# Performance work log

Measured on AMD Instinct MI355X. Metric: run time of the kernel, lower is better.

## Reference

```python
import jax, jax.numpy as jnp
import numpy as np

QMAX = 255.0  # bit=8 unsigned activation range


def ste_round(x):
    # straight-through round: exact integer rounding in fwd, identity grad
    return x + jax.lax.stop_gradient(jnp.round(x) - x)


def conv3x3(x, w, stride=1):
    return jax.lax.conv_general_dilated(
        x, w, window_strides=(stride, stride), padding=((1, 1), (1, 1)),
        dimension_numbers=('NCHW', 'OIHW', 'NCHW'))


def setup_inputs() -> dict:
    key = jax.random.key(0)
    k0, k1, k2 = jax.random.split(key, 3)
    N, C, H, W = 64, 256, 28, 28
    # uint8 activations and int8 (symmetric) weights, stored as integer-valued fp32
    x = jax.random.randint(k0, (N, C, H, W), 0, 256).astype(jnp.float32)
    w1 = jax.random.randint(k1, (C, C, 3, 3), -128, 128).astype(jnp.float32)
    w2 = jax.random.randint(k2, (C, C, 3, 3), -128, 128).astype(jnp.float32)
    f = jnp.float32
    return dict(
        x=x, w1=w1, w2=w2,
        s_x=f(0.05), z_x=f(128.0),
        s_w1=f(0.01), s_conv1=f(0.08), z_conv1=f(120.0),
        s_w2=f(0.01), s_conv2=f(0.07), z_conv2=f(130.0),
        s_add=f(0.09), z_add=f(125.0))


def qconv(x_q, w_q, s_in, z_in, s_w, s_out, z_out, stride=1):
    # integer-arithmetic conv: sum((x - z_in) * w) then requantize
    acc = conv3x3(x_q - z_in, w_q, stride)
    M = s_in * s_w / s_out  # per-cluster requant multiplier (cluster 0)
    return jnp.clip(ste_round(M * acc) + z_out, 0.0, QMAX)


def qadd(a, s_a, z_a, b, s_b, z_b, s_out, z_out):
    # fused dequant of both branches + residual add + requant
    y = (s_a / s_out) * (a - z_a) + (s_b / s_out) * (b - z_b)
    return jnp.clip(ste_round(y) + z_out, 0.0, QMAX)


def reference(x, w1, w2, s_x, z_x, s_w1, s_conv1, z_conv1,
              s_w2, s_conv2, z_conv2, s_add, z_add):
    out = qconv(x, w1, s_x, z_x, s_w1, s_conv1, z_conv1)          # conv1
    out = qconv(out, w2, s_conv1, z_conv1, s_w2, s_conv2, z_conv2)  # conv2
    return qadd(x, s_x, z_x, out, s_conv2, z_conv2, s_add, z_add)   # shortcut
```

## Files before the change

kernel.cpp:

```cpp
#include <hip/hip_runtime.h>
#include <stdint.h>

#define HWP 784
#define NPOS 50176
#define PLN ((size_t)NPOS * 64)
#define SLAB_ROWS 186
#define NCHUNK 2976
#define PAD_OFF 47616

typedef int   int4v   __attribute__((ext_vector_type(4)));
typedef int   int16v  __attribute__((ext_vector_type(16)));
typedef float float4v __attribute__((ext_vector_type(4)));
using as1_cv = const __attribute__((address_space(1))) void;
using as3_v  = __attribute__((address_space(3))) void;

__global__ __launch_bounds__(256) void k_nhwc(const float* __restrict__ x,
                                              int8_t* __restrict__ x8) {
    __shared__ int lA[256 * 15];
    __shared__ __align__(16) int lB[56 * 68];
    const int tid = threadIdx.x;
    const int P0 = blockIdx.x * 56;
    const int n = P0 / HWP;
    const int hw0 = P0 % HWP;
    const float* xb = x + (size_t)n * 256 * HWP + hw0;
#pragma unroll
    for (int k = 0; k < 14; ++k) {
        int e = tid + k * 256;
        int c = e / 14, pq = e % 14;
        float4v v = *(const float4v*)(xb + (size_t)c * HWP + pq * 4);
        int b0 = ((int)v[0] - 128) & 255;
        int b1 = ((int)v[1] - 128) & 255;
        int b2 = ((int)v[2] - 128) & 255;
        int b3 = ((int)v[3] - 128) & 255;
        lA[c * 15 + pq] = b0 | (b1 << 8) | (b2 << 16) | (b3 << 24);
    }
    __syncthreads();
#pragma unroll
    for (int k = 0; k < 4; ++k) {
        int u = tid + k * 256;
        if (u < 896) {
            int cg = u / 14, pq = u % 14;
            int d0 = lA[(cg * 4 + 0) * 15 + pq];
            int d1 = lA[(cg * 4 + 1) * 15 + pq];
            int d2 = lA[(cg * 4 + 2) * 15 + pq];
            int d3 = lA[(cg * 4 + 3) * 15 + pq];
#pragma unroll
            for (int j = 0; j < 4; ++j) {
                int sh = j * 8;
                int o = ((d0 >> sh) & 255) | (((d1 >> sh) & 255) << 8)
                      | (((d2 >> sh) & 255) << 16) | (((d3 >> sh) & 255) << 24);
                lB[(pq * 4 + j) * 68 + cg] = o;
            }
        }
    }
    __syncthreads();
#pragma unroll
    for (int k = 0; k < 4; ++k) {
        int ch = tid + k * 256;
        if (ch < 896) {
            int g = ch / 224, rem = ch % 224;
            int pos = rem >> 2, c4 = rem & 3;
            int4v val = *(const int4v*)&lB[pos * 68 + g * 16 + c4 * 4];
            *(int4v*)(x8 + (size_t)g * PLN + (size_t)(P0 + pos) * 64 + c4 * 16) = val;
        }
    }
}

__global__ __launch_bounds__(256) void k_w_prep(const float* __restrict__ wa,
                                                const float* __restrict__ wb,
                                                int8_t* __restrict__ w8a,
                                                int8_t* __restrict__ w8b,
                                                int* __restrict__ wsa,
                                                int* __restrict__ wsb) {
    __shared__ int red[256];
    const int which = blockIdx.x >> 8;
    const int oc = blockIdx.x & 255;
    const float* w = which ? wb : wa;
    int8_t* w8 = which ? w8b : w8a;
    int* wsum = which ? wsb : wsa;
    const int t = threadIdx.x;
    const float* src = w + (size_t)oc * 2304 + (size_t)t * 9;
    const int g = oc >> 5;
    const int l = ((t >> 4) & 1) * 32 + (oc & 31);
    const int j = t & 15;
    const int s2 = (t >> 5) & 1;
    const int kb = t >> 6;
    int acc = 0;
#pragma unroll
    for (int tap = 0; tap < 9; ++tap) {
        int wv = (int)src[tap];
        acc += wv;
        int oo = ((((tap * 4 + kb) * 2 + s2) * 8 + g) * 64 + l) * 16 + j;
        w8[oo] = (int8_t)wv;
    }
    red[t] = acc;
    __syncthreads();
    for (int st = 128; st > 0; st >>= 1) {
        if (t < st) red[t] += red[t + st];
        __syncthreads();
    }
    if (t == 0) wsum[oc] = red[0];
}

template<bool FUSED>
__global__ __launch_bounds__(256, 2) void k_qconv_t(const int8_t* __restrict__ in8,
        const int8_t* __restrict__ w8, const int* __restrict__ wsum,
        const float* __restrict__ s_in_p, const float* __restrict__ s_w_p,
        const float* __restrict__ s_out_p, const float* __restrict__ z_in_p,
        const float* __restrict__ z_out_p, int8_t* __restrict__ out8,
        const int8_t* __restrict__ x8, const float* __restrict__ sxp,
        const float* __restrict__ zxp, const float* __restrict__ sap,
        const float* __restrict__ zap, float* __restrict__ outf) {
    __shared__ __align__(16) int8_t slab[47872];
    const int tid = threadIdx.x;
    const int lane = tid & 63;
    const int half = lane >> 5;
    const int wv = tid >> 6;
    const int bid = blockIdx.x;
    const int tile = (bid & 7) * 49 + (bid >> 3);
    const int p0 = tile * 128;
    const int plane = wv;

#pragma unroll
    for (int k = 0; k < 12; ++k) {
        int chunkid = tid + k * 256;
        if (chunkid < NCHUNK) {
            int q = chunkid >> 4;
            int cs = chunkid & 15;
            int cg = cs ^ (q & 15);
            int qg = p0 - 29 + q;
            qg = qg < 0 ? 0 : (qg > NPOS - 1 ? NPOS - 1 : qg);
            const int8_t* src = in8 + (size_t)(cg >> 2) * PLN
                                    + (size_t)qg * 64 + (cg & 3) * 16;
            __builtin_amdgcn_global_load_lds((as1_cv*)src,
                                             (as3_v*)&slab[chunkid * 16], 16, 0, 0);
        }
    }

    const int zi = (int)z_in_p[0] - 128;
    const int spl = (zi & 0xff) * 0x01010101;
    if (tid < 16) {
        int4v pv; pv[0] = spl; pv[1] = spl; pv[2] = spl; pv[3] = spl;
        *(int4v*)&slab[PAD_OFF + tid * 16] = pv;
    }

    int rowpos[4], ph[4], pw[4];
#pragma unroll
    for (int mt = 0; mt < 4; ++mt) {
        rowpos[mt] = mt * 32 + (lane & 31);
        int p = p0 + rowpos[mt];
        int hw = p % HWP;
        ph[mt] = hw / 28;
        pw[mt] = hw % 28;
    }

    int16v acc[4][2];
#pragma unroll
    for (int mt = 0; mt < 4; ++mt)
#pragma unroll
        for (int nt = 0; nt < 2; ++nt)
#pragma unroll
            for (int r = 0; r < 16; ++r) acc[mt][nt][r] = 0;

    const int8_t* wlane = w8 + plane * 2048 + lane * 16;

    __syncthreads();

    int4v bc00 = *(const int4v*)(wlane);
    int4v bc10 = *(const int4v*)(wlane + 1024);
    int4v bc01 = *(const int4v*)(wlane + 8192);
    int4v bc11 = *(const int4v*)(wlane + 9216);

#pragma unroll
    for (int u = 0; u < 36; ++u) {
        const int tap = u >> 2, kb = u & 3;
        const int dh = tap / 3 - 1;
        const int dw = tap % 3 - 1;
        int4v bn00, bn10, bn01, bn11;
        if (u < 35) {
            const int8_t* wb_ = wlane + (size_t)(u + 1) * 16384;
            bn00 = *(const int4v*)(wb_);
            bn10 = *(const int4v*)(wb_ + 1024);
            bn01 = *(const int4v*)(wb_ + 8192);
            bn11 = *(const int4v*)(wb_ + 9216);
        }
        int4v a[4][2];
#pragma unroll
        for (int mt = 0; mt < 4; ++mt) {
            int q = rowpos[mt] + dh * 28 + dw + 29;
            bool ok = ((unsigned)(ph[mt] + dh) < 28u) & ((unsigned)(pw[mt] + dw) < 28u);
            int ab = (ok ? (q << 8) : PAD_OFF) ^ ((q & 15) << 4) ^ (half << 4);
            a[mt][0] = *(const int4v*)&slab[ab ^ ((kb * 4 + 0) << 4)];
            a[mt][1] = *(const int4v*)&slab[ab ^ ((kb * 4 + 2) << 4)];
        }
#pragma unroll
        for (int mt = 0; mt < 4; ++mt) {
            acc[mt][0] = __builtin_amdgcn_mfma_i32_32x32x32_i8(a[mt][0], bc00,
                                                               acc[mt][0], 0, 0, 0);
            acc[mt][1] = __builtin_amdgcn_mfma_i32_32x32x32_i8(a[mt][0], bc10,
                                                               acc[mt][1], 0, 0, 0);
        }
#pragma unroll
        for (int mt = 0; mt < 4; ++mt) {
            acc[mt][0] = __builtin_amdgcn_mfma_i32_32x32x32_i8(a[mt][1], bc01,
                                                               acc[mt][0], 0, 0, 0);
            acc[mt][1] = __builtin_amdgcn_mfma_i32_32x32x32_i8(a[mt][1], bc11,
                                                               acc[mt][1], 0, 0, 0);
        }
        bc00 = bn00; bc10 = bn10; bc01 = bn01; bc11 = bn11;
    }

    const float Mf = s_in_p[0] * s_w_p[0] / s_out_p[0];
    const float zof = z_out_p[0];
    const int zoffi = 128 - (int)z_in_p[0];

    if (!FUSED) {
        __syncthreads();
        int8_t* tpb = slab + wv * 10240;
#pragma unroll
        for (int mt = 0; mt < 4; ++mt)
#pragma unroll
            for (int nt = 0; nt < 2; ++nt) {
                int oc = plane * 64 + nt * 32 + (lane & 31);
                int corr = zoffi * wsum[oc];
#pragma unroll
                for (int r = 0; r < 16; ++r) {
                    int prow = (r & 3) + 8 * (r >> 2) + 4 * half;
                    int pl = mt * 32 + prow;
                    float q = rintf(Mf * (float)(acc[mt][nt][r] + corr)) + zof;
                    q = fminf(fmaxf(q, 0.0f), 255.0f);
                    tpb[pl * 80 + nt * 32 + (lane & 31)] = (int8_t)((int)q - 128);
                }
            }
#pragma unroll
        for (int h2 = 0; h2 < 2; ++h2) {
            const int rr = h2 * 64 + lane;
            int8_t* o8p = out8 + (size_t)plane * PLN + (size_t)(p0 + rr) * 64;
            const int8_t* rowp = tpb + rr * 80;
#pragma unroll
            for (int k = 0; k < 4; ++k)
                *(int4v*)(o8p + k * 16) = *(const int4v*)(rowp + k * 16);
        }
    } else {
        const float ra = sxp[0] / sap[0];
        const float rb = s_out_p[0] / sap[0];
        const float zx = zxp[0];
        const float z2 = z_out_p[0];
        const float za = zap[0];
        __syncthreads();
        float* tp = (float*)slab + wv * 2080;
        const int pl = lane & 31;
#pragma unroll
        for (int mt = 0; mt < 4; ++mt) {
#pragma unroll
            for (int nt = 0; nt < 2; ++nt) {
                int oc = plane * 64 + nt * 32 + (lane & 31);
                int corr = zoffi * wsum[oc];
#pragma unroll
                for (int r = 0; r < 16; ++r) {
                    int prow = (r & 3) + 8 * (r >> 2) + 4 * half;
                    float q2 = rintf(Mf * (float)(acc[mt][nt][r] + corr)) + zof;
                    q2 = fminf(fmaxf(q2, 0.0f), 255.0f);
                    tp[prow * 65 + nt * 32 + (lane & 31)] = q2;
                }
            }
            const int pglob = p0 + mt * 32 + pl;
            const int n = pglob / HWP;
            const int hwo = pglob % HWP;
            const int8_t* x8p = x8 + (size_t)plane * PLN + (size_t)pglob * 64 + half * 32;
            int4v r0 = *(const int4v*)x8p;
            int4v r1 = *(const int4v*)(x8p + 16);
            int xb[8];
            xb[0] = r0[0]; xb[1] = r0[1]; xb[2] = r0[2]; xb[3] = r0[3];
            xb[4] = r1[0]; xb[5] = r1[1]; xb[6] = r1[2]; xb[7] = r1[3];
            float* obase = outf + ((size_t)(n * 256 + plane * 64 + half * 32)) * HWP + hwo;
#pragma unroll
            for (int j = 0; j < 32; ++j) {
                int bv = (xb[j >> 2] >> ((j & 3) * 8)) & 255;
                int xval = (int)(int8_t)bv + 128;
                float q2 = tp[pl * 65 + half * 32 + j];
                float y = ra * ((float)xval - zx) + rb * (q2 - z2);
                float qf = rintf(y) + za;
                qf = fminf(fmaxf(qf, 0.0f), 255.0f);
                obase[(size_t)j * HWP] = qf;
            }
        }
    }
}

extern "C" void kernel_launch(void* const* d_in, const int* in_sizes, int n_in,
                              void* d_out, int out_size, void* d_ws, size_t ws_size,
                              hipStream_t stream) {
    (void)in_sizes; (void)n_in; (void)out_size; (void)ws_size;
    const float* x    = (const float*)d_in[0];
    const float* w1   = (const float*)d_in[1];
    const float* w2   = (const float*)d_in[2];
    const float* s_x  = (const float*)d_in[3];
    const float* z_x  = (const float*)d_in[4];
    const float* s_w1 = (const float*)d_in[5];
    const float* s_c1 = (const float*)d_in[6];
    const float* z_c1 = (const float*)d_in[7];
    const float* s_w2 = (const float*)d_in[8];
    const float* s_c2 = (const float*)d_in[9];
    const float* z_c2 = (const float*)d_in[10];
    const float* s_ad = (const float*)d_in[11];
    const float* z_ad = (const float*)d_in[12];
    float* out = (float*)d_out;

    int8_t* ws    = (int8_t*)d_ws;
    int8_t* x8    = ws;
    int8_t* o1    = ws + 12845056;
    int8_t* w8a   = ws + 25690112;
    int8_t* w8b   = ws + 26279936;
    int*    wsum1 = (int*)(ws + 26869760);
    int*    wsum2 = (int*)(ws + 26870784);

    k_nhwc<<<896, 256, 0, stream>>>(x, x8);
    k_w_prep<<<512, 256, 0, stream>>>(w1, w2, w8a, w8b, wsum1, wsum2);
    k_qconv_t<false><<<392, 256, 0, stream>>>(x8, w8a, wsum1,
        s_x, s_w1, s_c1, z_x, z_c1, o1,
        nullptr, nullptr, nullptr, nullptr, nullptr, nullptr);
    k_qconv_t<true><<<392, 256, 0, stream>>>(o1, w8b, wsum2,
        s_c1, s_w2, s_c2, z_c1, z_c2, nullptr,
        x8, s_x, z_x, s_ad, z_ad, out);
}
```

Before: 199.3 us.

## Double-buffer LDS A-fragments and interleave MFMAs with loads via sched_group_barrier

Loads the A operand fragments for the next tap/k-block from LDS one iteration ahead, alongside the already-prefetched weights. Explicit scheduling barriers interleave the MFMAs with the LDS reads. Launch bounds drop from two blocks per CU to one, which frees registers for the extra in-flight fragments. The cost is lower occupancy, so less latency hiding comes from running other waves.

```diff
diff --git a/kernel.cpp b/kernel.cpp
--- a/kernel.cpp
+++ b/kernel.cpp
@@ -13,6 +13,8 @@
 typedef float float4v __attribute__((ext_vector_type(4)));
 using as1_cv = const __attribute__((address_space(1))) void;
 using as3_v  = __attribute__((address_space(3))) void;
+
+#define SGB __builtin_amdgcn_sched_group_barrier
 
 __global__ __launch_bounds__(256) void k_nhwc(const float* __restrict__ x,
                                               int8_t* __restrict__ x8) {
@@ -103,7 +105,7 @@
 }
 
 template<bool FUSED>
-__global__ __launch_bounds__(256, 2) void k_qconv_t(const int8_t* __restrict__ in8,
+__global__ __launch_bounds__(256, 1) void k_qconv_t(const int8_t* __restrict__ in8,
         const int8_t* __restrict__ w8, const int* __restrict__ wsum,
         const float* __restrict__ s_in_p, const float* __restrict__ s_w_p,
         const float* __restrict__ s_out_p, const float* __restrict__ z_in_p,
@@ -170,44 +172,66 @@
     int4v bc10 = *(const int4v*)(wlane + 1024);
     int4v bc01 = *(const int4v*)(wlane + 8192);
     int4v bc11 = *(const int4v*)(wlane + 9216);
+    int4v ac[4][2];
+#pragma unroll
+    for (int mt = 0; mt < 4; ++mt) {
+        int q = rowpos[mt];
+        bool ok = ((unsigned)(ph[mt] - 1) < 28u) & ((unsigned)(pw[mt] - 1) < 28u);
+        int ab = (ok ? (q << 8) : PAD_OFF) ^ ((q & 15) << 4) ^ (half << 4);
+        ac[mt][0] = *(const int4v*)&slab[ab];
+        ac[mt][1] = *(const int4v*)&slab[ab ^ (2 << 4)];
+    }
 
 #pragma unroll
     for (int u = 0; u < 36; ++u) {
-        const int tap = u >> 2, kb = u & 3;
-        const int dh = tap / 3 - 1;
-        const int dw = tap % 3 - 1;
-        int4v bn00, bn10, bn01, bn11;
+        int4v an[4][2], bn00, bn10, bn01, bn11;
         if (u < 35) {
-            const int8_t* wb_ = wlane + (size_t)(u + 1) * 16384;
+            const int un = u + 1;
+            const int tapn = un >> 2, kbn = un & 3;
+            const int dhn = tapn / 3 - 1;
+            const int dwn = tapn % 3 - 1;
+            const int8_t* wb_ = wlane + (size_t)un * 16384;
             bn00 = *(const int4v*)(wb_);
             bn10 = *(const int4v*)(wb_ + 1024);
             bn01 = *(const int4v*)(wb_ + 8192);
             bn11 = *(const int4v*)(wb_ + 9216);
-        }
-        int4v a[4][2];
+#pragma unroll
+            for (int mt = 0; mt < 4; ++mt) {
+                int q = rowpos[mt] + dhn * 28 + dwn + 29;
+                bool ok = ((unsigned)(ph[mt] + dhn) < 28u)
+                        & ((unsigned)(pw[mt] + dwn) < 28u);
+                int ab = (ok ? (q << 8) : PAD_OFF) ^ ((q & 15) << 4) ^ (half << 4);
+                an[mt][0] = *(const int4v*)&slab[ab ^ ((kbn * 4 + 0) << 4)];
+                an[mt][1] = *(const int4v*)&slab[ab ^ ((kbn * 4 + 2) << 4)];
+            }
+        }
 #pragma unroll
         for (int mt = 0; mt < 4; ++mt) {
-            int q = rowpos[mt] + dh * 28 + dw + 29;
-            bool ok = ((unsigned)(ph[mt] + dh) < 28u) & ((unsigned)(pw[mt] + dw) < 28u);
-            int ab = (ok ? (q << 8) : PAD_OFF) ^ ((q & 15) << 4) ^ (half << 4);
-            a[mt][0] = *(const int4v*)&slab[ab ^ ((kb * 4 + 0) << 4)];
-            a[mt][1] = *(const int4v*)&slab[ab ^ ((kb * 4 + 2) << 4)];
+            acc[mt][0] = __builtin_amdgcn_mfma_i32_32x32x32_i8(ac[mt][0], bc00,
+                                                               acc[mt][0], 0, 0, 0);
+            acc[mt][1] = __builtin_amdgcn_mfma_i32_32x32x32_i8(ac[mt][0], bc10,
+                                                               acc[mt][1], 0, 0, 0);
         }
 #pragma unroll
         for (int mt = 0; mt < 4; ++mt) {
-            acc[mt][0] = __builtin_amdgcn_mfma_i32_32x32x32_i8(a[mt][0], bc00,
+            acc[mt][0] = __builtin_amdgcn_mfma_i32_32x32x32_i8(ac[mt][1], bc01,
                                                                acc[mt][0], 0, 0, 0);
-            acc[mt][1] = __builtin_amdgcn_mfma_i32_32x32x32_i8(a[mt][0], bc10,
+            acc[mt][1] = __builtin_amdgcn_mfma_i32_32x32x32_i8(ac[mt][1], bc11,
                                                                acc[mt][1], 0, 0, 0);
         }
-#pragma unroll
-        for (int mt = 0; mt < 4; ++mt) {
-            acc[mt][0] = __builtin_amdgcn_mfma_i32_32x32x32_i8(a[mt][1], bc01,
-                                                               acc[mt][0], 0, 0, 0);
-            acc[mt][1] = __builtin_amdgcn_mfma_i32_32x32x32_i8(a[mt][1], bc11,
-                                                               acc[mt][1], 0, 0, 0);
-        }
-        bc00 = bn00; bc10 = bn10; bc01 = bn01; bc11 = bn11;
+        if (u < 35) {
+            SGB(0x020, 4, 0);
+#pragma unroll
+            for (int g8 = 0; g8 < 8; ++g8) {
+                SGB(0x008, 2, 0);
+                SGB(0x100, 1, 0);
+            }
+#pragma unroll
+            for (int mt = 0; mt < 4; ++mt) {
+                ac[mt][0] = an[mt][0]; ac[mt][1] = an[mt][1];
+            }
+            bc00 = bn00; bc10 = bn10; bc01 = bn01; bc11 = bn11;
+        }
     }
 
     const float Mf = s_in_p[0] * s_w_p[0] / s_out_p[0];
```

New measurement: 232.6 us. +16.7%, slower.
